# Kernel optimization log

Measured on AMD Instinct MI355X. Metric: run time of the kernel, lower is better.

## Reference

```python
import jax, jax.numpy as jnp
import numpy as np


def conv2d(x, w, b=None):
    # NCHW conv, stride 1, 'same' padding inferred from kernel size
    ph, pw = w.shape[2] // 2, w.shape[3] // 2
    y = jax.lax.conv_general_dilated(
        x, w, window_strides=(1, 1), padding=[(ph, ph), (pw, pw)],
        dimension_numbers=('NCHW', 'OIHW', 'NCHW'))
    if b is not None:
        y = y + b[None, :, None, None]
    return y


def gelu(v):
    return jax.nn.gelu(v, approximate=False)  # torch nn.GELU default (erf)


def lrelu(v):
    return jnp.where(v >= 0, v, 0.1 * v)  # LeakyReLU(0.1)


def setup_inputs() -> dict:
    key = jax.random.key(0)
    ks = jax.random.split(key, 16)
    B, C, H, W = 2, 32, 256, 256
    s = 0.05
    return {
        'x':      jax.random.normal(ks[0], (B, C, H, W), jnp.float32),
        'key':    jax.random.normal(ks[1], (B, C, H, W), jnp.float32),
        'w_off1': jax.random.normal(ks[2], (32, 64, 3, 3), jnp.float32) * s,
        'b_off1': jax.random.normal(ks[3], (32,), jnp.float32) * s,
        'w_off2': jax.random.normal(ks[4], (32, 32, 3, 3), jnp.float32) * s,
        'b_off2': jax.random.normal(ks[5], (32,), jnp.float32) * s,
        'w_dcn':  jax.random.normal(ks[6], (288, 64, 3, 3), jnp.float32) * s,
        'b_dcn':  jax.random.normal(ks[7], (288,), jnp.float32) * s,
        'w_sel':  jax.random.normal(ks[8], (1, 3, 3, 3), jnp.float32) * s,
        'b_sel':  jax.random.normal(ks[9], (1,), jnp.float32) * s,
        'w_t1':   jax.random.normal(ks[10], (32, 32, 3, 3), jnp.float32) * s,
        'w_t2':   jax.random.normal(ks[11], (128, 32, 1, 1), jnp.float32) * s,
        'w_t3':   jax.random.normal(ks[12], (128, 128, 3, 3), jnp.float32) * s,
        'w_t4':   jax.random.normal(ks[13], (32, 128, 1, 1), jnp.float32) * s,
        'w_t5':   jax.random.normal(ks[14], (32, 32, 3, 3), jnp.float32) * s,
    }


def reference(x, key, w_off1, b_off1, w_off2, b_off2, w_dcn, b_dcn,
              w_sel, b_sel, w_t1, w_t2, w_t3, w_t4, w_t5):
    B, C, H, W = x.shape
    TOPK = 3
    # offset branch
    off = lrelu(conv2d(jnp.concatenate([x, key], axis=1), w_off1, b_off1))
    off = lrelu(conv2d(off, w_off2, b_off2))
    # dcn_attention proxy: conv over (key, offset) producing C*9 candidate warps
    warp = conv2d(jnp.concatenate([key, off], axis=1), w_dcn, b_dcn)
    warp = warp.reshape(B, C, 9, H, W)
    # correlation of each of 9 candidates with x, per pixel
    corr = jnp.einsum('bcohw,bchw->bohw', warp, x)            # [B,9,H,W]
    corr = corr.reshape(B, 9, H * W).transpose(0, 2, 1)       # [B,HW,9]
    _, idx = jax.lax.top_k(corr, TOPK)                        # [B,HW,3]
    # gather selected candidates per pixel per channel
    warp_p = warp.reshape(B, C, 9, H * W).transpose(0, 3, 2, 1)   # [B,HW,9,C]
    sel = jnp.take_along_axis(warp_p, idx[..., None], axis=2)     # [B,HW,3,C]
    key_warp = sel.reshape(B, H, W, TOPK, C).transpose(0, 4, 3, 1, 2)
    key_warp = key_warp.reshape(B * C, TOPK, H, W)
    key_warp = conv2d(key_warp, w_sel, b_sel).reshape(B, C, H, W)
    # tail: conv-GELU bottleneck stack
    y = conv2d(key_warp, w_t1)
    y = conv2d(gelu(y), w_t2)
    y = conv2d(gelu(y), w_t3)
    y = conv2d(gelu(y), w_t4)
    y = conv2d(gelu(y), w_t5)
    return y
```

## Files before the change

### kernel.cpp

```cpp
#include <hip/hip_runtime.h>
#include <math.h>

static constexpr int H = 256, W = 256, HW = H * W;
static constexpr int PW = 258, PREC = 66564;

typedef __attribute__((ext_vector_type(8))) _Float16 half8v;
typedef __attribute__((ext_vector_type(4))) _Float16 half4v;
typedef __attribute__((ext_vector_type(4))) float  float4v;

__device__ __forceinline__ half8v h8zero() {
  half8v z;
  #pragma unroll
  for (int i = 0; i < 8; ++i) z[i] = (_Float16)0;
  return z;
}

__device__ __forceinline__ void gload_lds16(const _Float16* g, _Float16* lds) {
  __builtin_amdgcn_global_load_lds(
      (const __attribute__((address_space(1))) void*)g,
      (__attribute__((address_space(3))) void*)lds, 16, 0, 0);
}

__device__ __forceinline__ float gelu_f(float v) {
  return 0.5f * v * (1.0f + erff(v * 0.70710678118654752440f));
}
template<int ACT>
__device__ __forceinline__ float apply_act(float v) {
  if constexpr (ACT == 1) return v >= 0.f ? v : 0.1f * v;
  if constexpr (ACT == 2) return gelu_f(v);
  return v;
}

__global__ __launch_bounds__(256)
void zero_border_k(_Float16* p0, _Float16* p1, _Float16* p2, _Float16* p3)
{
  int t = blockIdx.x * 256 + threadIdx.x;
  if (t >= 1028) return;
  int inst = blockIdx.y;
  _Float16* P = (inst >> 1) == 0 ? p0 : ((inst >> 1) == 1 ? p1 : ((inst >> 1) == 2 ? p2 : p3));
  int b = inst & 1;
  int y, x;
  if      (t < 258) { y = 0;          x = t; }
  else if (t < 516) { y = 257;        x = t - 258; }
  else if (t < 772) { y = t - 515;    x = 0; }
  else              { y = t - 771;    x = 257; }
  _Float16* o = P + (((size_t)b * PW + y) * PW + x) * 64;
  half8v z = h8zero();
  #pragma unroll
  for (int j = 0; j < 8; ++j) *(half8v*)&o[j * 8] = z;
}

__global__ __launch_bounds__(256)
void pack2_k(const float* __restrict__ inA, _Float16* __restrict__ pA,
             const float* __restrict__ inB, _Float16* __restrict__ pB)
{
  const int p = blockIdx.x * 256 + threadIdx.x;
  const int b = blockIdx.y;
  const float* in = blockIdx.z ? inB : inA;
  _Float16* P = blockIdx.z ? pB : pA;
  const float* ip = in + (size_t)b * 32 * HW + p;
  __attribute__((aligned(16))) _Float16 hv[32], lv[32];
  #pragma unroll
  for (int c = 0; c < 32; ++c) {
    float v = ip[(size_t)c * HW];
    _Float16 h = (_Float16)v;
    hv[c] = h;
    lv[c] = (_Float16)((v - (float)h) * 2048.0f);
  }
  const int y = p >> 8, xcol = p & 255;
  _Float16* o = P + (((size_t)b * PW + y + 1) * PW + xcol + 1) * 64;
  #pragma unroll
  for (int j = 0; j < 4; ++j) {
    *(half8v*)&o[j * 8]      = *(half8v*)&hv[j * 8];
    *(half8v*)&o[32 + j * 8] = *(half8v*)&lv[j * 8];
  }
}

__device__ __forceinline__ void prep_w_body(const float* w, _Float16* hi, _Float16* lo,
                                            int OC, int CIN, int tid)
{
  if (tid >= OC * CIN * 9) return;
  int ci = tid % CIN; int r = tid / CIN; int oc = r % OC; int tap = r / OC;
  float v = w[((size_t)oc * CIN + ci) * 9 + tap];
  _Float16 h = (_Float16)v;
  hi[tid] = h;
  lo[tid] = (_Float16)((v - (float)h) * 2048.0f);
}
__global__ __launch_bounds__(256)
void prep3_w_k(const float* __restrict__ w0, _Float16* __restrict__ h0, _Float16* __restrict__ l0, int OC0, int CIN0, int nb0,
               const float* __restrict__ w1, _Float16* __restrict__ h1, _Float16* __restrict__ l1, int OC1, int CIN1, int nb1,
               const float* __restrict__ w2, _Float16* __restrict__ h2, _Float16* __restrict__ l2, int OC2, int CIN2)
{
  int bb = blockIdx.x;
  if (bb < nb0)            prep_w_body(w0, h0, l0, OC0, CIN0, bb * 256 + threadIdx.x);
  else if (bb < nb0 + nb1) prep_w_body(w1, h1, l1, OC1, CIN1, (bb - nb0) * 256 + threadIdx.x);
  else                     prep_w_body(w2, h2, l2, OC2, CIN2, (bb - nb0 - nb1) * 256 + threadIdx.x);
}

template<int CIN, int OC, int OCB, int ACT, int OMODE, int SPLIT>
__global__ __launch_bounds__(256)
void conv3x3_mfma_k(const _Float16* __restrict__ iH0, const _Float16* __restrict__ iL0,
                    const _Float16* __restrict__ iH1, const _Float16* __restrict__ iL1, int cin0,
                    const _Float16* __restrict__ wHi, const _Float16* __restrict__ wLo,
                    const float* __restrict__ bias,
                    float* __restrict__ outF, _Float16* __restrict__ oH, _Float16* __restrict__ oL)
{
  constexpr int NOF  = OCB / 16;
  constexpr int NAQ  = (SPLIT == 3) ? NOF : 1;
  constexpr int REC  = (SPLIT == 3) ? 64 : 32;
  constexpr int nOcg = OC / OCB;
  __shared__ _Float16 sB[6 * 66 * REC];

  const int l  = threadIdx.x & 63;
  const int wv = threadIdx.x >> 6;

  const int bid = blockIdx.x;
  const int xcd = bid & 7, q = bid >> 3;
  const int ocg  = q % nOcg;
  const int tIdx = (q / nOcg) * 8 + xcd;
  const int b   = tIdx >> 8;
  const int x0  = ((tIdx >> 6) & 3) * 64;
  const int y0  = (tIdx & 63) * 4;
  const int oc0 = ocg * OCB;

  float4v accP[NOF][4];
  float4v accQ[NAQ][4];
  #pragma unroll
  for (int j = 0; j < NOF; ++j)
    #pragma unroll
    for (int f = 0; f < 4; ++f)
      accP[j][f] = (float4v){0.f, 0.f, 0.f, 0.f};
  #pragma unroll
  for (int j = 0; j < NAQ; ++j)
    #pragma unroll
    for (int f = 0; f < 4; ++f)
      accQ[j][f] = (float4v){0.f, 0.f, 0.f, 0.f};

  const int k8  = (l >> 4) * 8;
  const int ocl = l & 15;
  const int rowy = y0 + wv;
  const int sq  = l & 3;
  const int spx = l >> 2;

  #pragma unroll 1
  for (int cc = 0; cc < CIN; cc += 32) {
    if constexpr (SPLIT == 3) {
      const _Float16* cb = (cc < cin0 ? iH0 : iH1) + (size_t)b * ((size_t)PREC * 64);
      __syncthreads();
      #pragma unroll
      for (int k = 0; k < 12; ++k) {
        int t = wv + 4 * k;
        int r = t >> 3, s = t & 7;
        const _Float16* src = cb
            + (((size_t)(y0 + r) * PW) + (x0 + s * 8 + (l >> 3))) * 64
            + ((l & 7) ^ (l >> 3)) * 8;
        gload_lds16(src, &sB[(r * 66 + s * 8) * 64]);
      }
      #pragma unroll
      for (int rr = wv; rr < 6; rr += 4) {
        if (l < 16) {
          int pxo = l >> 3;
          int slot = l & 7;
          const _Float16* src = cb
              + (((size_t)(y0 + rr) * PW) + (x0 + 64 + pxo)) * 64 + (slot ^ pxo) * 8;
          half8v v = *(const half8v*)src;
          *(half8v*)&sB[(rr * 66 + 64 + pxo) * 64 + slot * 8] = v;
        }
      }
      __syncthreads();
    } else {
      const _Float16* cbH;
      {
        size_t o = (size_t)(b * (CIN >> 5) + (cc >> 5)) * HW * 32;
        cbH = iH0 + o;
      }
      __syncthreads();
      #pragma unroll 2
      for (int t = wv; t < 30; t += 4) {
        int r = t / 5; int s = t - r * 5;
        int gy = y0 + r - 1;
        bool vy = (gy >= 0) && (gy < H);
        int gyc = gy < 0 ? 0 : (gy >= H ? H - 1 : gy);
        int pxl = s * 16 + spx;
        bool lact = (s < 4) || (l < 8);
        int gx = x0 + pxl - 1;
        bool vx = (gx >= 0) && (gx < W);
        int gxc = gx < 0 ? 0 : (gx >= W ? W - 1 : gx);
        half8v v = h8zero();
        if (lact && vy && vx)
          v = *(const half8v*)&cbH[((size_t)gyc * W + gxc) * 32 + sq * 8];
        int cls = (sq ^ pxl) & 3;
        if (lact)
          *(half8v*)&sB[(r * 66 + pxl) * 32 + cls * 8] = v;
      }
      __syncthreads();
    }

    #pragma unroll 1
    for (int tap = 0; tap < 9; ++tap) {
      const int dy = tap / 3, dx = tap - 3 * (tap / 3);
      half8v ah[NOF], aq[NAQ];
      const _Float16* hp = wHi + ((size_t)tap * OC + oc0 + ocl) * CIN + cc + k8;
      #pragma unroll
      for (int j = 0; j < NOF; ++j)
        ah[j] = *(const half8v*)(hp + (size_t)j * 16 * CIN);
      if constexpr (SPLIT == 3) {
        const _Float16* lp = wLo + ((size_t)tap * OC + oc0 + ocl) * CIN + cc + k8;
        #pragma unroll
        for (int j = 0; j < NOF; ++j)
          aq[j] = *(const half8v*)(lp + (size_t)j * 16 * CIN);
      }
      const int px = ocl + dx;
      if constexpr (SPLIT == 3) {
        const int rbase = ((wv + dy) * 66 + px) * 64;
        const int clsH = (l >> 4) ^ (px & 7);
        const int clsQ = ((l >> 4) + 4) ^ (px & 7);
        __builtin_amdgcn_s_setprio(1);
        #pragma unroll
        for (int f = 0; f < 4; ++f) {
          half8v bh = *(const half8v*)&sB[rbase + f * 1024 + clsH * 8];
          half8v bq = *(const half8v*)&sB[rbase + f * 1024 + clsQ * 8];
          #pragma unroll
          for (int j = 0; j < NOF; ++j) {
            accP[j][f] = __builtin_amdgcn_mfma_f32_16x16x32_f16(ah[j], bh, accP[j][f], 0, 0, 0);
            accQ[j][f] = __builtin_amdgcn_mfma_f32_16x16x32_f16(ah[j], bq, accQ[j][f], 0, 0, 0);
            accQ[j][f] = __builtin_amdgcn_mfma_f32_16x16x32_f16(aq[j], bh, accQ[j][f], 0, 0, 0);
          }
        }
        __builtin_amdgcn_s_setprio(0);
      } else {
        const int rbase = ((wv + dy) * 66 + px) * 32;
        const int clsH = ((l >> 4) ^ px) & 3;
        __builtin_amdgcn_s_setprio(1);
        #pragma unroll
        for (int f = 0; f < 4; ++f) {
          half8v bh = *(const half8v*)&sB[rbase + f * 512 + clsH * 8];
          #pragma unroll
          for (int j = 0; j < NOF; ++j)
            accP[j][f] = __builtin_amdgcn_mfma_f32_16x16x32_f16(ah[j], bh, accP[j][f], 0, 0, 0);
        }
        __builtin_amdgcn_s_setprio(0);
      }
    }
  }

  #pragma unroll
  for (int j = 0; j < NOF; ++j)
    #pragma unroll
    for (int f = 0; f < 4; ++f) {
      const int px  = x0 + f * 16 + ocl;
      const int occ = oc0 + j * 16 + (l >> 4) * 4;
      float vv4[4];
      #pragma unroll
      for (int r = 0; r < 4; ++r) {
        float bv = bias ? bias[occ + r] : 0.f;
        float vv = accP[j][f][r] + bv;
        if constexpr (SPLIT == 3) vv += accQ[j][f][r] * (1.0f / 2048.0f);
        vv4[r] = apply_act<ACT>(vv);
      }
      if constexpr (OMODE == 0) {
        #pragma unroll
        for (int r = 0; r < 4; ++r)
          outF[((size_t)(b * OC + occ + r) * H + rowy) * W + px] = vv4[r];
      } else if constexpr (OMODE == 1) {
        __attribute__((aligned(8))) _Float16 hv[4], lv[4];
        #pragma unroll
        for (int r = 0; r < 4; ++r) {
          _Float16 h = (_Float16)vv4[r];
          hv[r] = h;
          lv[r] = (_Float16)((vv4[r] - (float)h) * 2048.0f);
        }
        size_t rec = ((size_t)b * PW + rowy + 1) * PW + px + 1;
        *(half4v*)&oH[rec * 64 + occ]      = *(half4v*)&hv[0];
        *(half4v*)&oH[rec * 64 + 32 + occ] = *(half4v*)&lv[0];
      } else {
        __attribute__((aligned(8))) _Float16 hv[4];
        #pragma unroll
        for (int r = 0; r < 4; ++r) hv[r] = (_Float16)vv4[r];
        size_t ob = ((size_t)b * HW + (size_t)rowy * W + px) * OC + occ;
        *(half4v*)&oH[ob] = *(half4v*)&hv[0];
      }
    }
}

template<int CIN, int OCB, int ACT>
__global__ __launch_bounds__(256)
void conv1x1_nhwc_k(const _Float16* __restrict__ in, const float* __restrict__ w,
                    _Float16* __restrict__ oH, int OC)
{
  __shared__ __align__(16) float sW[OCB][CIN];
  const int b   = blockIdx.y;
  const int oc0 = blockIdx.z * OCB;
  for (int t = threadIdx.x; t < OCB * CIN; t += 256)
    sW[t / CIN][t % CIN] = w[(size_t)(oc0 + t / CIN) * CIN + (t % CIN)];
  __syncthreads();

  const int pb = blockIdx.x * 1024 + threadIdx.x;
  float acc[OCB][4];
  #pragma unroll
  for (int o = 0; o < OCB; ++o)
    #pragma unroll
    for (int i = 0; i < 4; ++i) acc[o][i] = 0.f;

  #pragma unroll 1
  for (int c0 = 0; c0 < CIN; c0 += 8) {
    float v[4][8];
    #pragma unroll
    for (int i = 0; i < 4; ++i) {
      const _Float16* ip = in + ((size_t)b * HW + pb + i * 256) * CIN + c0;
      half8v hv8 = *(const half8v*)ip;
      #pragma unroll
      for (int j = 0; j < 8; ++j) v[i][j] = (float)hv8[j];
    }
    #pragma unroll
    for (int o = 0; o < OCB; ++o) {
      const float4 w0 = *(const float4*)&sW[o][c0];
      const float4 w1 = *(const float4*)&sW[o][c0 + 4];
      #pragma unroll
      for (int i = 0; i < 4; ++i) {
        acc[o][i] += v[i][0]*w0.x + v[i][1]*w0.y + v[i][2]*w0.z + v[i][3]*w0.w
                   + v[i][4]*w1.x + v[i][5]*w1.y + v[i][6]*w1.z + v[i][7]*w1.w;
      }
    }
  }
  #pragma unroll
  for (int i = 0; i < 4; ++i) {
    __attribute__((aligned(16))) _Float16 hv[OCB];
    #pragma unroll
    for (int o = 0; o < OCB; ++o)
      hv[o] = (_Float16)apply_act<ACT>(acc[o][i]);
    size_t ob = ((size_t)(b * (OC >> 5) + (oc0 >> 5)) * HW + pb + i * 256) * 32 + (oc0 & 31);
    #pragma unroll
    for (int j = 0; j < OCB / 8; ++j)
      *(half8v*)&oH[ob + j * 8] = *(half8v*)&hv[j * 8];
  }
}

__global__ __launch_bounds__(256)
void corr_topk_k(const float* __restrict__ warp, const float* __restrict__ x,
                 int* __restrict__ idxo)
{
  const int p2 = (blockIdx.x * 256 + threadIdx.x) * 2;
  const int b = blockIdx.y;
  float corr[9][2];
  #pragma unroll
  for (int o = 0; o < 9; ++o) { corr[o][0] = 0.f; corr[o][1] = 0.f; }
  #pragma unroll 1
  for (int c = 0; c < 32; ++c) {
    float2 xv = *(const float2*)&x[((size_t)b * 32 + c) * HW + p2];
    const float* wp = warp + ((size_t)b * 288 + (size_t)c * 9) * HW + p2;
    #pragma unroll
    for (int o = 0; o < 9; ++o) {
      float2 wv = *(const float2*)&wp[(size_t)o * HW];
      corr[o][0] += wv.x * xv.x;
      corr[o][1] += wv.y * xv.y;
    }
  }
  int2 packs;
  #pragma unroll
  for (int i = 0; i < 2; ++i) {
    unsigned mask = 0;
    int packed = 0;
    #pragma unroll
    for (int t = 0; t < 3; ++t) {
      float best = -INFINITY; int bi = 0;
      #pragma unroll
      for (int o = 0; o < 9; ++o) {
        bool take = (((mask >> o) & 1u) == 0u) && (corr[o][i] > best);
        best = take ? corr[o][i] : best;
        bi   = take ? o          : bi;
      }
      mask   |= 1u << bi;
      packed |= bi << (4 * t);
    }
    ((int*)&packs)[i] = packed;
  }
  *(int2*)&idxo[(size_t)b * HW + p2] = packs;
}

__global__ __launch_bounds__(256)
void selconv_k(const float* __restrict__ warp, const int* __restrict__ idxp,
               const float* __restrict__ wsel, const float* __restrict__ bsel,
               _Float16* __restrict__ oH)
{
  const int tx = threadIdx.x & 31, ty = threadIdx.x >> 5;
  const int px = blockIdx.x * 32 + tx;
  const int py = blockIdx.y * 8 + ty;
  const int b  = blockIdx.z;

  int  nidx[9];
  bool nval[9];
  int  qoff[9];
  #pragma unroll
  for (int kh = 0; kh < 3; ++kh)
    #pragma unroll
    for (int kw = 0; kw < 3; ++kw) {
      int k = kh * 3 + kw;
      int qy = py + kh - 1, qx = px + kw - 1;
      nval[k] = (qy >= 0 && qy < H && qx >= 0 && qx < W);
      qoff[k] = qy * W + qx;
      nidx[k] = nval[k] ? idxp[(size_t)b * HW + qoff[k]] : 0;
    }

  float ws27[27];
  #pragma unroll
  for (int i = 0; i < 27; ++i) ws27[i] = wsel[i];
  const float bs = bsel[0];

  float arr[32];
  #pragma unroll 1
  for (int c = 0; c < 32; ++c) {
    float acc = bs;
    const float* wb = warp + ((size_t)b * 288 + (size_t)c * 9) * HW;
    #pragma unroll
    for (int k = 0; k < 9; ++k) {
      if (nval[k]) {
        int pk = nidx[k];
        #pragma unroll
        for (int t = 0; t < 3; ++t) {
          int o = (pk >> (4 * t)) & 15;
          acc += ws27[t * 9 + k] * wb[(size_t)o * HW + qoff[k]];
        }
      }
    }
    arr[c] = acc;
  }

  __attribute__((aligned(16))) _Float16 hv[32];
  #pragma unroll
  for (int c = 0; c < 32; ++c) hv[c] = (_Float16)arr[c];
  size_t ob = ((size_t)b * HW + (size_t)py * W + px) * 32;
  #pragma unroll
  for (int j = 0; j < 4; ++j)
    *(half8v*)&oH[ob + j * 8] = *(half8v*)&hv[j * 8];
}

extern "C" void kernel_launch(void* const* d_in, const int* in_sizes, int n_in,
                              void* d_out, int out_size, void* d_ws, size_t ws_size,
                              hipStream_t stream) {
  const float* x      = (const float*)d_in[0];
  const float* key    = (const float*)d_in[1];
  const float* w_off1 = (const float*)d_in[2];
  const float* b_off1 = (const float*)d_in[3];
  const float* w_off2 = (const float*)d_in[4];
  const float* b_off2 = (const float*)d_in[5];
  const float* w_dcn  = (const float*)d_in[6];
  const float* b_dcn  = (const float*)d_in[7];
  const float* w_sel  = (const float*)d_in[8];
  const float* b_sel  = (const float*)d_in[9];
  const float* w_t1   = (const float*)d_in[10];
  const float* w_t2   = (const float*)d_in[11];
  const float* w_t3   = (const float*)d_in[12];
  const float* w_t4   = (const float*)d_in[13];
  const float* w_t5   = (const float*)d_in[14];

  char* ws = (char*)d_ws;
  float* warp = (float*)(ws);
  _Float16* xP   = (_Float16*)(ws);
  _Float16* o1P  = (_Float16*)(ws + 17040384);
  _Float16* w1H  = (_Float16*)(ws + 34080768);
  _Float16* w1L  = w1H + 18432;
  _Float16* w2H  = w1L + 18432;
  _Float16* w2L  = w2H + 9216;
  _Float16* wdH  = (_Float16*)(ws + 150994944);
  _Float16* wdL  = wdH + 165888;
  _Float16* keyP = (_Float16*)(ws + 151658496);
  _Float16* o2P  = (_Float16*)(ws + 168698880);
  int*      idxb = (int*)(ws + 150994944);
  _Float16* kwH  = (_Float16*)(ws + 151658496);
  _Float16* twB  = (_Float16*)(ws + 160047104);
  _Float16* t1H_w = twB;
  _Float16* t1L_w = twB + 9216;
  _Float16* t3H_w = twB + 18432;
  _Float16* t3L_w = twB + 165888;
  _Float16* t5H_w = twB + 313344;
  _Float16* t5L_w = twB + 322560;
  _Float16* y1  = (_Float16*)(ws);
  _Float16* t2H = (_Float16*)(ws + 16777216);
  _Float16* t4H = (_Float16*)(ws + 50331648);
  _Float16* y3  = (_Float16*)(ws + 83886080);
  float* out = (float*)d_out;

  dim3 blk(256);

  zero_border_k<<<dim3(5, 8), blk, 0, stream>>>(xP, keyP, o1P, o2P);
  pack2_k<<<dim3(256, 2, 2), blk, 0, stream>>>(x, xP, key, keyP);
  prep3_w_k<<<dim3(756), blk, 0, stream>>>(
      w_off1, w1H, w1L, 32, 64, 72,
      w_off2, w2H, w2L, 32, 32, 36,
      w_dcn,  wdH, wdL, 288, 64);

  conv3x3_mfma_k<64, 32, 32, 1, 1, 3><<<dim3(512), blk, 0, stream>>>(
      xP, nullptr, keyP, nullptr, 32, w1H, w1L, b_off1, nullptr, o1P, nullptr);
  conv3x3_mfma_k<32, 32, 32, 1, 1, 3><<<dim3(512), blk, 0, stream>>>(
      o1P, nullptr, nullptr, nullptr, 32, w2H, w2L, b_off2, nullptr, o2P, nullptr);
  conv3x3_mfma_k<64, 288, 32, 0, 0, 3><<<dim3(4608), blk, 0, stream>>>(
      keyP, nullptr, o2P, nullptr, 32, wdH, wdL, b_dcn, warp, nullptr, nullptr);
  corr_topk_k<<<dim3(128, 2), blk, 0, stream>>>(warp, x, idxb);
  selconv_k<<<dim3(8, 32, 2), blk, 0, stream>>>(warp, idxb, w_sel, b_sel, kwH);

  prep3_w_k<<<dim3(648), blk, 0, stream>>>(
      w_t1, t1H_w, t1L_w, 32, 32, 36,
      w_t3, t3H_w, t3L_w, 128, 128, 576,
      w_t5, t5H_w, t5L_w, 32, 32);

  conv3x3_mfma_k<32, 32, 32, 2, 3, 1><<<dim3(512), blk, 0, stream>>>(
      kwH, nullptr, nullptr, nullptr, 32, t1H_w, t1L_w, nullptr, nullptr, y1, nullptr);
  conv1x1_nhwc_k<32, 16, 2><<<dim3(64, 2, 8), blk, 0, stream>>>(y1, w_t2, t2H, 128);
  conv3x3_mfma_k<128, 128, 64, 2, 3, 1><<<dim3(1024), blk, 0, stream>>>(
      t2H, nullptr, nullptr, nullptr, 128, t3H_w, t3L_w, nullptr, nullptr, y3, nullptr);
  conv1x1_nhwc_k<128, 16, 2><<<dim3(64, 2, 2), blk, 0, stream>>>(y3, w_t4, t4H, 32);
  conv3x3_mfma_k<32, 32, 32, 0, 0, 1><<<dim3(512), blk, 0, stream>>>(
      t4H, nullptr, nullptr, nullptr, 32, t5H_w, t5L_w, nullptr, out, nullptr, nullptr);
}
```

Before: 606.0 us.

## Use zero-padded NHWC buffers for tail convs and async LDS loads

The producers of the tail conv inputs (selconv and the 1x1 convs) now write into zero-bordered padded 258x258 records. Small kernels are added to zero the borders. The single-split 3x3 conv path can then drop its bounds-checked, clamped halo gather and use global_load_lds direct-to-LDS copies with an XOR swizzle, as the split path already does. This trades three extra small border-zeroing launches and slightly larger buffers for simpler, asynchronous tile loads in the tail convolutions.

```diff
diff --git a/kernel.cpp b/kernel.cpp
--- a/kernel.cpp
+++ b/kernel.cpp
@@ -2,7 +2,8 @@
 #include <math.h>
 
 static constexpr int H = 256, W = 256, HW = H * W;
-static constexpr int PW = 258, PREC = 66564;
+static constexpr int PW = 258;
+static constexpr size_t PREC = 66564;
 
 typedef __attribute__((ext_vector_type(8))) _Float16 half8v;
 typedef __attribute__((ext_vector_type(4))) _Float16 half4v;
@@ -32,7 +33,7 @@
 }
 
 __global__ __launch_bounds__(256)
-void zero_border_k(_Float16* p0, _Float16* p1, _Float16* p2, _Float16* p3)
+void zero_border64_k(_Float16* p0, _Float16* p1, _Float16* p2, _Float16* p3)
 {
   int t = blockIdx.x * 256 + threadIdx.x;
   if (t >= 1028) return;
@@ -40,14 +41,40 @@
   _Float16* P = (inst >> 1) == 0 ? p0 : ((inst >> 1) == 1 ? p1 : ((inst >> 1) == 2 ? p2 : p3));
   int b = inst & 1;
   int y, x;
-  if      (t < 258) { y = 0;          x = t; }
-  else if (t < 516) { y = 257;        x = t - 258; }
-  else if (t < 772) { y = t - 515;    x = 0; }
-  else              { y = t - 771;    x = 257; }
-  _Float16* o = P + (((size_t)b * PW + y) * PW + x) * 64;
+  if      (t < 258) { y = 0;        x = t; }
+  else if (t < 516) { y = 257;      x = t - 258; }
+  else if (t < 772) { y = t - 515;  x = 0; }
+  else              { y = t - 771;  x = 257; }
+  _Float16* o = P + ((size_t)b * PREC + (size_t)y * PW + x) * 64;
   half8v z = h8zero();
   #pragma unroll
   for (int j = 0; j < 8; ++j) *(half8v*)&o[j * 8] = z;
+}
+
+__global__ __launch_bounds__(256)
+void zero_border32_k(_Float16* p0, size_t s0, _Float16* p1, size_t s1,
+                     _Float16* p2, size_t s2, _Float16* p3, size_t s3)
+{
+  int t = blockIdx.x * 256 + threadIdx.x;
+  if (t >= 1028) return;
+  int inst = blockIdx.y;
+  _Float16* P; size_t bs;
+  switch (inst >> 1) {
+    case 0: P = p0; bs = s0; break;
+    case 1: P = p1; bs = s1; break;
+    case 2: P = p2; bs = s2; break;
+    default: P = p3; bs = s3; break;
+  }
+  int b = inst & 1;
+  int y, x;
+  if      (t < 258) { y = 0;        x = t; }
+  else if (t < 516) { y = 257;      x = t - 258; }
+  else if (t < 772) { y = t - 515;  x = 0; }
+  else              { y = t - 771;  x = 257; }
+  _Float16* o = P + ((size_t)b * bs + (size_t)y * PW + x) * 32;
+  half8v z = h8zero();
+  #pragma unroll
+  for (int j = 0; j < 4; ++j) *(half8v*)&o[j * 8] = z;
 }
 
 __global__ __launch_bounds__(256)
@@ -68,7 +95,7 @@
     lv[c] = (_Float16)((v - (float)h) * 2048.0f);
   }
   const int y = p >> 8, xcol = p & 255;
-  _Float16* o = P + (((size_t)b * PW + y + 1) * PW + xcol + 1) * 64;
+  _Float16* o = P + ((size_t)b * PREC + (size_t)(y + 1) * PW + xcol + 1) * 64;
   #pragma unroll
   for (int j = 0; j < 4; ++j) {
     *(half8v*)&o[j * 8]      = *(half8v*)&hv[j * 8];
@@ -139,13 +166,11 @@
   const int k8  = (l >> 4) * 8;
   const int ocl = l & 15;
   const int rowy = y0 + wv;
-  const int sq  = l & 3;
-  const int spx = l >> 2;
 
   #pragma unroll 1
   for (int cc = 0; cc < CIN; cc += 32) {
     if constexpr (SPLIT == 3) {
-      const _Float16* cb = (cc < cin0 ? iH0 : iH1) + (size_t)b * ((size_t)PREC * 64);
+      const _Float16* cb = (cc < cin0 ? iH0 : iH1) + (size_t)b * (PREC * 64);
       __syncthreads();
       #pragma unroll
       for (int k = 0; k < 12; ++k) {
@@ -159,8 +184,7 @@
       #pragma unroll
       for (int rr = wv; rr < 6; rr += 4) {
         if (l < 16) {
-          int pxo = l >> 3;
-          int slot = l & 7;
+          int pxo = l >> 3, slot = l & 7;
           const _Float16* src = cb
               + (((size_t)(y0 + rr) * PW) + (x0 + 64 + pxo)) * 64 + (slot ^ pxo) * 8;
           half8v v = *(const half8v*)src;
@@ -169,29 +193,26 @@
       }
       __syncthreads();
     } else {
-      const _Float16* cbH;
-      {
-        size_t o = (size_t)(b * (CIN >> 5) + (cc >> 5)) * HW * 32;
-        cbH = iH0 + o;
-      }
+      const _Float16* cb = iH0 + (size_t)(b * (CIN >> 5) + (cc >> 5)) * (PREC * 32);
       __syncthreads();
-      #pragma unroll 2
-      for (int t = wv; t < 30; t += 4) {
-        int r = t / 5; int s = t - r * 5;
-        int gy = y0 + r - 1;
-        bool vy = (gy >= 0) && (gy < H);
-        int gyc = gy < 0 ? 0 : (gy >= H ? H - 1 : gy);
-        int pxl = s * 16 + spx;
-        bool lact = (s < 4) || (l < 8);
-        int gx = x0 + pxl - 1;
-        bool vx = (gx >= 0) && (gx < W);
-        int gxc = gx < 0 ? 0 : (gx >= W ? W - 1 : gx);
-        half8v v = h8zero();
-        if (lact && vy && vx)
-          v = *(const half8v*)&cbH[((size_t)gyc * W + gxc) * 32 + sq * 8];
-        int cls = (sq ^ pxl) & 3;
-        if (lact)
-          *(half8v*)&sB[(r * 66 + pxl) * 32 + cls * 8] = v;
+      #pragma unroll
+      for (int k = 0; k < 6; ++k) {
+        int t = wv + 4 * k;
+        int r = t >> 2, s = t & 3;
+        const _Float16* src = cb
+            + (((size_t)(y0 + r) * PW) + (x0 + s * 16 + (l >> 2))) * 32
+            + ((l & 3) ^ ((l >> 2) & 3)) * 8;
+        gload_lds16(src, &sB[(r * 66 + s * 16) * 32]);
+      }
+      #pragma unroll
+      for (int rr = wv; rr < 6; rr += 4) {
+        if (l < 8) {
+          int pxo = l >> 2, slot = l & 3;
+          const _Float16* src = cb
+              + (((size_t)(y0 + rr) * PW) + (x0 + 64 + pxo)) * 32 + (slot ^ pxo) * 8;
+          half8v v = *(const half8v*)src;
+          *(half8v*)&sB[(rr * 66 + 64 + pxo) * 32 + slot * 8] = v;
+        }
       }
       __syncthreads();
     }
@@ -270,7 +291,7 @@
           hv[r] = h;
           lv[r] = (_Float16)((vv4[r] - (float)h) * 2048.0f);
         }
-        size_t rec = ((size_t)b * PW + rowy + 1) * PW + px + 1;
+        size_t rec = (size_t)b * PREC + (size_t)(rowy + 1) * PW + px + 1;
         *(half4v*)&oH[rec * 64 + occ]      = *(half4v*)&hv[0];
         *(half4v*)&oH[rec * 64 + 32 + occ] = *(half4v*)&lv[0];
       } else {
@@ -286,7 +307,7 @@
 template<int CIN, int OCB, int ACT>
 __global__ __launch_bounds__(256)
 void conv1x1_nhwc_k(const _Float16* __restrict__ in, const float* __restrict__ w,
-                    _Float16* __restrict__ oH, int OC)
+                    _Float16* __restrict__ oP, int OC)
 {
   __shared__ __align__(16) float sW[OCB][CIN];
   const int b   = blockIdx.y;
@@ -329,10 +350,12 @@
     #pragma unroll
     for (int o = 0; o < OCB; ++o)
       hv[o] = (_Float16)apply_act<ACT>(acc[o][i]);
-    size_t ob = ((size_t)(b * (OC >> 5) + (oc0 >> 5)) * HW + pb + i * 256) * 32 + (oc0 & 31);
+    int p = pb + i * 256;
+    int y = p >> 8, xcol = p & 255;
+    size_t rec = (size_t)(b * (OC >> 5) + (oc0 >> 5)) * PREC + (size_t)(y + 1) * PW + xcol + 1;
     #pragma unroll
     for (int j = 0; j < OCB / 8; ++j)
-      *(half8v*)&oH[ob + j * 8] = *(half8v*)&hv[j * 8];
+      *(half8v*)&oP[rec * 32 + (oc0 & 31) + j * 8] = *(half8v*)&hv[j * 8];
   }
 }
 
@@ -381,7 +404,7 @@
 __global__ __launch_bounds__(256)
 void selconv_k(const float* __restrict__ warp, const int* __restrict__ idxp,
                const float* __restrict__ wsel, const float* __restrict__ bsel,
-               _Float16* __restrict__ oH)
+               _Float16* __restrict__ oP)
 {
   const int tx = threadIdx.x & 31, ty = threadIdx.x >> 5;
   const int px = blockIdx.x * 32 + tx;
@@ -429,10 +452,10 @@
   __attribute__((aligned(16))) _Float16 hv[32];
   #pragma unroll
   for (int c = 0; c < 32; ++c) hv[c] = (_Float16)arr[c];
-  size_t ob = ((size_t)b * HW + (size_t)py * W + px) * 32;
+  size_t rec = (size_t)b * PREC + (size_t)(py + 1) * PW + px + 1;
   #pragma unroll
   for (int j = 0; j < 4; ++j)
-    *(half8v*)&oH[ob + j * 8] = *(half8v*)&hv[j * 8];
+    *(half8v*)&oP[rec * 32 + j * 8] = *(half8v*)&hv[j * 8];
 }
 
 extern "C" void kernel_launch(void* const* d_in, const int* in_sizes, int n_in,
@@ -467,8 +490,8 @@
   _Float16* keyP = (_Float16*)(ws + 151658496);
   _Float16* o2P  = (_Float16*)(ws + 168698880);
   int*      idxb = (int*)(ws + 150994944);
-  _Float16* kwH  = (_Float16*)(ws + 151658496);
-  _Float16* twB  = (_Float16*)(ws + 160047104);
+  _Float16* kwP  = (_Float16*)(ws + 151658496);
+  _Float16* twB  = (_Float16*)(ws + 160178688);
   _Float16* t1H_w = twB;
   _Float16* t1L_w = twB + 9216;
   _Float16* t3H_w = twB + 18432;
@@ -476,14 +499,14 @@
   _Float16* t5H_w = twB + 313344;
   _Float16* t5L_w = twB + 322560;
   _Float16* y1  = (_Float16*)(ws);
-  _Float16* t2H = (_Float16*)(ws + 16777216);
-  _Float16* t4H = (_Float16*)(ws + 50331648);
+  _Float16* t2P = (_Float16*)(ws + 16777216);
+  _Float16* t4P = (_Float16*)(ws + 58720256);
   _Float16* y3  = (_Float16*)(ws + 83886080);
   float* out = (float*)d_out;
 
   dim3 blk(256);
 
-  zero_border_k<<<dim3(5, 8), blk, 0, stream>>>(xP, keyP, o1P, o2P);
+  zero_border64_k<<<dim3(5, 8), blk, 0, stream>>>(xP, keyP, o1P, o2P);
   pack2_k<<<dim3(256, 2, 2), blk, 0, stream>>>(x, xP, key, keyP);
   prep3_w_k<<<dim3(756), blk, 0, stream>>>(
       w_off1, w1H, w1L, 32, 64, 72,
@@ -497,19 +520,23 @@
   conv3x3_mfma_k<64, 288, 32, 0, 0, 3><<<dim3(4608), blk, 0, stream>>>(
       keyP, nullptr, o2P, nullptr, 32, wdH, wdL, b_dcn, warp, nullptr, nullptr);
   corr_topk_k<<<dim3(128, 2), blk, 0, stream>>>(warp, x, idxb);
-  selconv_k<<<dim3(8, 32, 2), blk, 0, stream>>>(warp, idxb, w_sel, b_sel, kwH);
-
+  zero_border32_k<<<dim3(5, 2), blk, 0, stream>>>(kwP, PREC, kwP, PREC, kwP, PREC, kwP, PREC);
+  selconv_k<<<dim3(8, 32, 2), blk, 0, stream>>>(warp, idxb, w_sel, b_sel, kwP);
+
+  zero_border32_k<<<dim3(5, 8), blk, 0, stream>>>(
+      t2P, 4 * PREC, t2P + PREC * 32, 4 * PREC, t2P + 2 * PREC * 32, 4 * PREC, t2P + 3 * PREC * 32, 4 * PREC);
+  zero_border32_k<<<dim3(5, 2), blk, 0, stream>>>(t4P, PREC, t4P, PREC, t4P, PREC, t4P, PREC);
   prep3_w_k<<<dim3(648), blk, 0, stream>>>(
       w_t1, t1H_w, t1L_w, 32, 32, 36,
       w_t3, t3H_w, t3L_w, 128, 128, 576,
       w_t5, t5H_w, t5L_w, 32, 32);
 
   conv3x3_mfma_k<32, 32, 32, 2, 3, 1><<<dim3(512), blk, 0, stream>>>(
-      kwH, nullptr, nullptr, nullptr, 32, t1H_w, t1L_w, nullptr, nullptr, y1, nullptr);
-  conv1x1_nhwc_k<32, 16, 2><<<dim3(64, 2, 8), blk, 0, stream>>>(y1, w_t2, t2H, 128);
+      kwP, nullptr, nullptr, nullptr, 32, t1H_w, t1L_w, nullptr, nullptr, y1, nullptr);
+  conv1x1_nhwc_k<32, 16, 2><<<dim3(64, 2, 8), blk, 0, stream>>>(y1, w_t2, t2P, 128);
   conv3x3_mfma_k<128, 128, 64, 2, 3, 1><<<dim3(1024), blk, 0, stream>>>(
-      t2H, nullptr, nullptr, nullptr, 128, t3H_w, t3L_w, nullptr, nullptr, y3, nullptr);
-  conv1x1_nhwc_k<128, 16, 2><<<dim3(64, 2, 2), blk, 0, stream>>>(y3, w_t4, t4H, 32);
+      t2P, nullptr, nullptr, nullptr, 128, t3H_w, t3L_w, nullptr, nullptr, y3, nullptr);
+  conv1x1_nhwc_k<128, 16, 2><<<dim3(64, 2, 2), blk, 0, stream>>>(y3, w_t4, t4P, 32);
   conv3x3_mfma_k<32, 32, 32, 0, 0, 1><<<dim3(512), blk, 0, stream>>>(
-      t4H, nullptr, nullptr, nullptr, 32, t5H_w, t5L_w, nullptr, out, nullptr, nullptr);
-}
+      t4P, nullptr, nullptr, nullptr, 32, t5H_w, t5L_w, nullptr, out, nullptr, nullptr);
+}
```

Measured after the change: 600.8 us (median of 2 runs). Within noise of the previous version (-0.9%).
